# Kernel optimization log

Hardware: AMD Instinct MI355X
Metric: run time of the kernel (lower is better)

## Reference

```python
import jax, jax.numpy as jnp
import numpy as np

LATENT = 64
HID = 64
IN_DIM = HID + 1  # 65
SLOPE = 0.2
EPS = 1e-8


def setup_inputs() -> dict:
    key = jax.random.key(0)
    ks = jax.random.split(key, 9)
    x = jax.random.normal(ks[0], (8192, LATENT, IN_DIM), dtype=jnp.float32)
    def init_w(k, shape, fan_in):
        return jax.random.uniform(k, shape, jnp.float32, -1.0, 1.0) / np.sqrt(fan_in)
    # Per-latent stacked MLP params: 3 LeakyReLU layers + final linear to scalar
    W0 = init_w(ks[1], (LATENT, HID, IN_DIM), IN_DIM)
    b0 = init_w(ks[2], (LATENT, HID), IN_DIM)
    W1 = init_w(ks[3], (LATENT, HID, HID), HID)
    b1 = init_w(ks[4], (LATENT, HID), HID)
    W2 = init_w(ks[5], (LATENT, HID, HID), HID)
    b2 = init_w(ks[6], (LATENT, HID), HID)
    W3 = init_w(ks[7], (LATENT, 1, HID), HID)
    b3 = init_w(ks[8], (LATENT, 1), HID)
    return {"x": x, "W0": W0, "b0": b0, "W1": W1, "b1": b1,
            "W2": W2, "b2": b2, "W3": W3, "b3": b3}


def _flow_single(w0, b0, w1, b1, w2, b2, w3, b3, xi):
    # xi: [B, IN_DIM] -> residual [B], d(out)/d(xi[:, -1]) [B]
    def f(z):
        h = jax.nn.leaky_relu(z @ w0.T + b0, SLOPE)
        h = jax.nn.leaky_relu(h @ w1.T + b1, SLOPE)
        h = jax.nn.leaky_relu(h @ w2.T + b2, SLOPE)
        return h @ w3.T + b3  # [B, 1]
    # only the last column of the Jacobian is used -> single batched JVP
    tan = jnp.zeros_like(xi).at[:, -1].set(1.0)
    out, dout = jax.jvp(f, (xi,), (tan,))
    return out[:, 0], dout[:, 0]


def reference(x, W0, b0, W1, b1, W2, b2, W3, b3):
    B = x.shape[0]
    # vmap over the latent axis (independent MLP per latent)
    residuals, dJ = jax.vmap(_flow_single,
                             in_axes=(0, 0, 0, 0, 0, 0, 0, 0, 1),
                             out_axes=(1, 1))(W0, b0, W1, b1, W2, b2, W3, b3, x)
    # residuals: [B, LATENT]; dJ: [B, LATENT]
    logabsdet = jnp.sum(jnp.log(jnp.abs(dJ) + EPS), axis=1)  # [B]
    return residuals.reshape(B, -1), logabsdet.reshape(B, -1)
```

## Files before the change

kernel.cpp:

```cpp
#include <hip/hip_runtime.h>
#include <hip/hip_bf16.h>
#include <cmath>

#define LATENTS 64
#define HID 64
#define IN_DIM 65
#define SLOPE 0.2f
#define FEPS 1e-8f
#define RPB 128
#define WBYTES 53248
#define W65_BYTE (64 * WBYTES)

#define A_OF_SLOT(s) ((((((s) >> 2) & 1) * 2 + ((s) >> 5)) * 16) + ((((s) >> 3) & 3) * 4) + ((s) & 3))

typedef __attribute__((ext_vector_type(8))) short short8;
typedef __attribute__((ext_vector_type(4))) float f32x4;
typedef __attribute__((address_space(1))) const unsigned GASU;
typedef __attribute__((address_space(3))) unsigned LASU;

__device__ __forceinline__ unsigned asu(float f){ return __builtin_bit_cast(unsigned, f); }
__device__ __forceinline__ float    asf(unsigned u){ return __builtin_bit_cast(float, u); }
__device__ __forceinline__ unsigned bfu(float f){
    return (unsigned)__builtin_bit_cast(unsigned short, __float2bfloat16(f));
}

__device__ __forceinline__ void split8v(const float* f, short8& hi, short8& lo){
    unsigned hw[4], lw[4];
#pragma unroll
    for (int w = 0; w < 4; ++w){
        float a = f[2 * w], b = f[2 * w + 1];
        unsigned ha = asu(a) & 0xFFFF0000u, hb = asu(b) & 0xFFFF0000u;
        float la = a - asf(ha), lb = b - asf(hb);
        hw[w] = (ha >> 16) | hb;
        lw[w] = bfu(la) | (bfu(lb) << 16);
    }
    uint4 h4{hw[0], hw[1], hw[2], hw[3]}, l4{lw[0], lw[1], lw[2], lw[3]};
    hi = __builtin_bit_cast(short8, h4);
    lo = __builtin_bit_cast(short8, l4);
}

__device__ __forceinline__ void split8t(const float* f, short8& hi, short8& lo){
    unsigned hw[4], lw[4];
#pragma unroll
    for (int w = 0; w < 4; ++w){
        float a = f[2 * w], b = f[2 * w + 1];
        unsigned ha = asu(a) & 0xFFFF0000u, hb = asu(b) & 0xFFFF0000u;
        float la = a - asf(ha), lb = b - asf(hb);
        hw[w] = __builtin_amdgcn_perm(asu(b),  asu(a),  0x07060302u);
        lw[w] = __builtin_amdgcn_perm(asu(lb), asu(la), 0x07060302u);
    }
    uint4 h4{hw[0], hw[1], hw[2], hw[3]}, l4{lw[0], lw[1], lw[2], lw[3]};
    hi = __builtin_bit_cast(short8, h4);
    lo = __builtin_bit_cast(short8, l4);
}

__device__ __forceinline__ short8 pack8t(const float* f){
    unsigned w[4];
#pragma unroll
    for (int i = 0; i < 4; ++i)
        w[i] = __builtin_amdgcn_perm(asu(f[2 * i + 1]), asu(f[2 * i]), 0x07060302u);
    uint4 p{w[0], w[1], w[2], w[3]};
    return __builtin_bit_cast(short8, p);
}

__device__ __forceinline__ f32x4 mfma_(short8 a, short8 b, f32x4 c){
    return __builtin_amdgcn_mfma_f32_16x16x32_bf16(a, b, c, 0, 0, 0);
}

__global__ void lad_init_kernel(float* __restrict__ lad, int n){
    int i = blockIdx.x * blockDim.x + threadIdx.x;
    if (i < n) lad[i] = 0.0f;
}

__global__ __launch_bounds__(64)
void w_prep_kernel(const float* __restrict__ W0, const float* __restrict__ W1,
                   const float* __restrict__ W2, const float* __restrict__ W3,
                   char* __restrict__ ws)
{
    const int b = blockIdx.x;
    const int L = threadIdx.x;
    const int c  = L & 15;
    const int kb = (L >> 4) * 8;
    if (b < 192){
        const int l = b / 3, d = b - 3 * l;
        const float* Wd = (d == 0) ? W0 + (size_t)l * 64 * IN_DIM
                        : (d == 1) ? W1 + (size_t)l * 4096
                                   : W2 + (size_t)l * 4096;
        const int K = (d == 0) ? IN_DIM : 64;
#pragma unroll
        for (int ks = 0; ks < 2; ++ks)
#pragma unroll
            for (int ct = 0; ct < 4; ++ct){
                float wf[8];
#pragma unroll
                for (int j = 0; j < 8; ++j){
                    const int s = ks * 32 + kb + j;
                    const int a = (d == 0) ? s : A_OF_SLOT(s);
                    wf[j] = Wd[(size_t)(ct * 16 + c) * K + a];
                }
                short8 wh, wl;
                split8v(wf, wh, wl);
                char* base = ws + (size_t)l * WBYTES + d * 16384 + (ks * 4 + ct) * 1024 + L * 16;
                *(short8*)base            = wh;
                *(short8*)(base + 8192)   = wl;
            }
    } else {
        const int l = b - 192;
#pragma unroll
        for (int ks = 0; ks < 2; ++ks){
            float wf[8];
#pragma unroll
            for (int j = 0; j < 8; ++j)
                wf[j] = (c == 0) ? W3[l * 64 + A_OF_SLOT(ks * 32 + kb + j)] : 0.0f;
            short8 wh, wl;
            split8v(wf, wh, wl);
            char* base = ws + (size_t)l * WBYTES + 49152 + ks * 1024 + L * 16;
            *(short8*)base          = wh;
            *(short8*)(base + 2048) = wl;
        }
        ((float*)(ws + W65_BYTE))[l * 64 + L] =
            W0[(size_t)l * 64 * IN_DIM + L * IN_DIM + 64];
    }
}

__global__ __launch_bounds__(512, 4)
void flow_mfma_kernel(const float* __restrict__ x,
                      const float* __restrict__ b0, const float* __restrict__ b1,
                      const float* __restrict__ b2, const float* __restrict__ b3,
                      const char* __restrict__ ws,
                      float* __restrict__ out_res, float* __restrict__ out_lad)
{
    __shared__ __attribute__((aligned(16))) char wlds[WBYTES];

    const int l   = blockIdx.y;
    const int tid = threadIdx.x;
    const int L   = tid & 63;
    const int wv  = tid >> 6;
    const int u   = L >> 4;
    const int g0  = blockIdx.x * RPB + wv * 16 + (L & 15);

    const char* gsrc = ws + (size_t)l * WBYTES;
#pragma unroll
    for (int i = 0; i < 7; ++i){
        const int base = i * 512 + wv * 64;
        if (base * 16 < WBYTES)
            __builtin_amdgcn_global_load_lds((GASU*)(gsrc + (base + L) * 16),
                                             (LASU*)(wlds + base * 16), 16, 0, 0);
    }

    const float* xg0 = x + ((size_t)g0 * LATENTS + l) * IN_DIM;
    float xv[16];
    float x65r;
#pragma unroll
    for (int j = 0; j < 8; ++j){
        xv[j]     = xg0[8 * u + j];
        xv[8 + j] = xg0[32 + 8 * u + j];
    }
    x65r = xg0[64];

    short8 bh[2], bl2[2], th2[2];
    split8t(&xv[0], bh[0], bl2[0]);
    split8t(&xv[8], bh[1], bl2[1]);

    __syncthreads();

    f32x4 ha[4], ta[4];

    auto ldw = [&](int d, int ks, int ct, short8& wh, short8& wl){
        const char* p = wlds + d * 16384 + (ks * 4 + ct) * 1024 + (L << 4);
        wh = *(const short8*)p;
        wl = *(const short8*)(p + 8192);
    };
    auto repack = [&](const float v[4][4], short8 (&hi)[2], short8 (&lo)[2]){
#pragma unroll
        for (int ks = 0; ks < 2; ++ks){
            float f8[8] = {v[ks][0], v[ks][1], v[ks][2], v[ks][3],
                           v[2 + ks][0], v[2 + ks][1], v[2 + ks][2], v[2 + ks][3]};
            split8t(f8, hi[ks], lo[ks]);
        }
    };
    auto repackt = [&](const float v[4][4], short8 (&hi)[2]){
#pragma unroll
        for (int ks = 0; ks < 2; ++ks){
            float f8[8] = {v[ks][0], v[ks][1], v[ks][2], v[ks][3],
                           v[2 + ks][0], v[2 + ks][1], v[2 + ks][2], v[2 + ks][3]};
            hi[ks] = pack8t(f8);
        }
    };

    {
#pragma unroll
        for (int ct = 0; ct < 4; ++ct)
            ha[ct] = __builtin_bit_cast(f32x4,
                        *(const float4*)(b0 + l * 64 + ct * 16 + u * 4));
#pragma unroll
        for (int ks = 0; ks < 2; ++ks){
#pragma unroll
            for (int ct = 0; ct < 4; ++ct){
                short8 wh, wl;
                ldw(0, ks, ct, wh, wl);
                __builtin_amdgcn_s_setprio(1);
                ha[ct] = mfma_(wh, bh[ks],  ha[ct]);
                ha[ct] = mfma_(wh, bl2[ks], ha[ct]);
                ha[ct] = mfma_(wl, bh[ks],  ha[ct]);
                __builtin_amdgcn_s_setprio(0);
            }
        }
        const float* w65p = (const float*)(ws + W65_BYTE) + l * 64;
        float hv[4][4], tv[4][4];
#pragma unroll
        for (int ct = 0; ct < 4; ++ct){
            const float4 wv4 = *(const float4*)(w65p + ct * 16 + u * 4);
            const float wa[4] = {wv4.x, wv4.y, wv4.z, wv4.w};
#pragma unroll
            for (int i = 0; i < 4; ++i){
                float z = fmaf(x65r, wa[i], ha[ct][i]);
                float m = (z >= 0.0f) ? 1.0f : SLOPE;
                hv[ct][i] = z * m;
                tv[ct][i] = wa[i] * m;
            }
        }
        repack(hv, bh, bl2);
        repackt(tv, th2);
    }

    auto dense2 = [&](int d, const float* __restrict__ bl){
#pragma unroll
        for (int ct = 0; ct < 4; ++ct){
            ha[ct] = __builtin_bit_cast(f32x4,
                        *(const float4*)(bl + ct * 16 + u * 4));
            ta[ct] = (f32x4){0.f, 0.f, 0.f, 0.f};
        }
#pragma unroll
        for (int ks = 0; ks < 2; ++ks){
#pragma unroll
            for (int ct = 0; ct < 4; ++ct){
                short8 wh, wl;
                ldw(d, ks, ct, wh, wl);
                __builtin_amdgcn_s_setprio(1);
                ha[ct] = mfma_(wh, bh[ks],  ha[ct]);
                ha[ct] = mfma_(wh, bl2[ks], ha[ct]);
                ha[ct] = mfma_(wl, bh[ks],  ha[ct]);
                ta[ct] = mfma_(wh, th2[ks], ta[ct]);
                ta[ct] = mfma_(wl, th2[ks], ta[ct]);
                __builtin_amdgcn_s_setprio(0);
            }
        }
        float hv[4][4], tv[4][4];
#pragma unroll
        for (int ct = 0; ct < 4; ++ct)
#pragma unroll
            for (int i = 0; i < 4; ++i){
                float z  = ha[ct][i];
                float zt = ta[ct][i];
                float m  = (z >= 0.0f) ? 1.0f : SLOPE;
                hv[ct][i] = z * m;
                tv[ct][i] = zt * m;
            }
        repack(hv, bh, bl2);
        repackt(tv, th2);
    };
    dense2(1, b1 + l * 64);
    dense2(2, b2 + l * 64);

    {
        f32x4 so = (f32x4){0.f, 0.f, 0.f, 0.f};
        f32x4 sd = (f32x4){0.f, 0.f, 0.f, 0.f};
#pragma unroll
        for (int ks = 0; ks < 2; ++ks){
            const char* p = wlds + 49152 + ks * 1024 + (L << 4);
            short8 wh = *(const short8*)p;
            short8 wl = *(const short8*)(p + 2048);
            __builtin_amdgcn_s_setprio(1);
            so = mfma_(wh, bh[ks],  so);
            so = mfma_(wh, bl2[ks], so);
            so = mfma_(wl, bh[ks],  so);
            sd = mfma_(wh, th2[ks], sd);
            sd = mfma_(wl, th2[ks], sd);
            __builtin_amdgcn_s_setprio(0);
        }
        if (u == 0){
            out_res[(size_t)g0 * LATENTS + l] = so[0] + b3[l];
            atomicAdd(&out_lad[g0], __logf(fabsf(sd[0]) + FEPS));
        }
    }
}

extern "C" void kernel_launch(void* const* d_in, const int* in_sizes, int n_in,
                              void* d_out, int out_size, void* d_ws, size_t ws_size,
                              hipStream_t stream)
{
    const float* x  = (const float*)d_in[0];
    const float* W0 = (const float*)d_in[1];
    const float* b0 = (const float*)d_in[2];
    const float* W1 = (const float*)d_in[3];
    const float* b1 = (const float*)d_in[4];
    const float* W2 = (const float*)d_in[5];
    const float* b2 = (const float*)d_in[6];
    const float* W3 = (const float*)d_in[7];
    const float* b3 = (const float*)d_in[8];

    const int B = in_sizes[0] / (LATENTS * IN_DIM);
    float* out_res = (float*)d_out;
    float* out_lad = out_res + (size_t)B * LATENTS;
    char*  wsp     = (char*)d_ws;

    lad_init_kernel<<<dim3((B + 255) / 256), dim3(256), 0, stream>>>(out_lad, B);
    w_prep_kernel<<<dim3(256), dim3(64), 0, stream>>>(W0, W1, W2, W3, wsp);
    flow_mfma_kernel<<<dim3(B / RPB, LATENTS), dim3(512), 0, stream>>>(
        x, b0, b1, b2, b3, wsp, out_res, out_lad);
}
```

Before: 73.85 us.

## Loop each block over several row chunks and drop tangent low-part MFMAs

Each block now loads its latent's weights into LDS once and then processes 8 chunks of 128 rows in a loop, so the grid shrinks by 8x and the per-block weight staging is amortized. The tangent path now uses a single round-to-nearest bf16 operand instead of a hi/lo split, which removes one MFMA per tile in the hidden and output layers. The split helpers also switch to rounding rather than truncation. The cost is less parallelism (512 blocks in total) and a small loss of tangent precision, which could affect the log-determinant accuracy.

Result: slower. 75.42 us (+2.1%).

```diff
diff --git a/kernel.cpp b/kernel.cpp
--- a/kernel.cpp
+++ b/kernel.cpp
@@ -8,6 +8,7 @@
 #define SLOPE 0.2f
 #define FEPS 1e-8f
 #define RPB 128
+#define CHUNKS 8
 #define WBYTES 53248
 #define W65_BYTE (64 * WBYTES)
 
@@ -29,9 +30,9 @@
 #pragma unroll
     for (int w = 0; w < 4; ++w){
         float a = f[2 * w], b = f[2 * w + 1];
-        unsigned ha = asu(a) & 0xFFFF0000u, hb = asu(b) & 0xFFFF0000u;
-        float la = a - asf(ha), lb = b - asf(hb);
-        hw[w] = (ha >> 16) | hb;
+        unsigned ua = bfu(a), ub = bfu(b);
+        float la = a - asf(ua << 16), lb = b - asf(ub << 16);
+        hw[w] = ua | (ub << 16);
         lw[w] = bfu(la) | (bfu(lb) << 16);
     }
     uint4 h4{hw[0], hw[1], hw[2], hw[3]}, l4{lw[0], lw[1], lw[2], lw[3]};
@@ -44,21 +45,22 @@
 #pragma unroll
     for (int w = 0; w < 4; ++w){
         float a = f[2 * w], b = f[2 * w + 1];
-        unsigned ha = asu(a) & 0xFFFF0000u, hb = asu(b) & 0xFFFF0000u;
-        float la = a - asf(ha), lb = b - asf(hb);
-        hw[w] = __builtin_amdgcn_perm(asu(b),  asu(a),  0x07060302u);
-        lw[w] = __builtin_amdgcn_perm(asu(lb), asu(la), 0x07060302u);
+        float la = a - asf(asu(a) & 0xFFFF0000u);
+        float lb = b - asf(asu(b) & 0xFFFF0000u);
+        hw[w] = __builtin_amdgcn_perm(asu(b), asu(a), 0x07060302u);
+        lw[w] = __builtin_amdgcn_perm(asu(lb) + 0x8000u, asu(la) + 0x8000u, 0x07060302u);
     }
     uint4 h4{hw[0], hw[1], hw[2], hw[3]}, l4{lw[0], lw[1], lw[2], lw[3]};
     hi = __builtin_bit_cast(short8, h4);
     lo = __builtin_bit_cast(short8, l4);
 }
 
-__device__ __forceinline__ short8 pack8t(const float* f){
+__device__ __forceinline__ short8 pack8r(const float* f){
     unsigned w[4];
 #pragma unroll
     for (int i = 0; i < 4; ++i)
-        w[i] = __builtin_amdgcn_perm(asu(f[2 * i + 1]), asu(f[2 * i]), 0x07060302u);
+        w[i] = __builtin_amdgcn_perm(asu(f[2 * i + 1]) + 0x8000u,
+                                     asu(f[2 * i])     + 0x8000u, 0x07060302u);
     uint4 p{w[0], w[1], w[2], w[3]};
     return __builtin_bit_cast(short8, p);
 }
@@ -137,7 +139,6 @@
     const int L   = tid & 63;
     const int wv  = tid >> 6;
     const int u   = L >> 4;
-    const int g0  = blockIdx.x * RPB + wv * 16 + (L & 15);
 
     const char* gsrc = ws + (size_t)l * WBYTES;
 #pragma unroll
@@ -147,141 +148,143 @@
             __builtin_amdgcn_global_load_lds((GASU*)(gsrc + (base + L) * 16),
                                              (LASU*)(wlds + base * 16), 16, 0, 0);
     }
-
-    const float* xg0 = x + ((size_t)g0 * LATENTS + l) * IN_DIM;
-    float xv[16];
-    float x65r;
-#pragma unroll
-    for (int j = 0; j < 8; ++j){
-        xv[j]     = xg0[8 * u + j];
-        xv[8 + j] = xg0[32 + 8 * u + j];
-    }
-    x65r = xg0[64];
-
-    short8 bh[2], bl2[2], th2[2];
-    split8t(&xv[0], bh[0], bl2[0]);
-    split8t(&xv[8], bh[1], bl2[1]);
-
     __syncthreads();
-
-    f32x4 ha[4], ta[4];
 
     auto ldw = [&](int d, int ks, int ct, short8& wh, short8& wl){
         const char* p = wlds + d * 16384 + (ks * 4 + ct) * 1024 + (L << 4);
         wh = *(const short8*)p;
         wl = *(const short8*)(p + 8192);
     };
-    auto repack = [&](const float v[4][4], short8 (&hi)[2], short8 (&lo)[2]){
-#pragma unroll
-        for (int ks = 0; ks < 2; ++ks){
-            float f8[8] = {v[ks][0], v[ks][1], v[ks][2], v[ks][3],
-                           v[2 + ks][0], v[2 + ks][1], v[2 + ks][2], v[2 + ks][3]};
-            split8t(f8, hi[ks], lo[ks]);
+
+#pragma unroll 1
+    for (int it = 0; it < CHUNKS; ++it){
+        const int g0 = (blockIdx.x * CHUNKS + it) * RPB + wv * 16 + (L & 15);
+
+        const float* xg0 = x + ((size_t)g0 * LATENTS + l) * IN_DIM;
+        float xv[16];
+#pragma unroll
+        for (int j = 0; j < 8; ++j){
+            xv[j]     = xg0[8 * u + j];
+            xv[8 + j] = xg0[32 + 8 * u + j];
         }
-    };
-    auto repackt = [&](const float v[4][4], short8 (&hi)[2]){
-#pragma unroll
-        for (int ks = 0; ks < 2; ++ks){
-            float f8[8] = {v[ks][0], v[ks][1], v[ks][2], v[ks][3],
-                           v[2 + ks][0], v[2 + ks][1], v[2 + ks][2], v[2 + ks][3]};
-            hi[ks] = pack8t(f8);
+        const float x65r = xg0[64];
+
+        short8 bh[2], bl2[2], th2[2];
+        split8t(&xv[0], bh[0], bl2[0]);
+        split8t(&xv[8], bh[1], bl2[1]);
+
+        f32x4 ha[4], ta[4];
+
+        auto repack = [&](const float v[4][4], short8 (&hi)[2], short8 (&lo)[2]){
+#pragma unroll
+            for (int ks = 0; ks < 2; ++ks){
+                float f8[8] = {v[ks][0], v[ks][1], v[ks][2], v[ks][3],
+                               v[2 + ks][0], v[2 + ks][1], v[2 + ks][2], v[2 + ks][3]};
+                split8t(f8, hi[ks], lo[ks]);
+            }
+        };
+        auto repackt = [&](const float v[4][4], short8 (&hi)[2]){
+#pragma unroll
+            for (int ks = 0; ks < 2; ++ks){
+                float f8[8] = {v[ks][0], v[ks][1], v[ks][2], v[ks][3],
+                               v[2 + ks][0], v[2 + ks][1], v[2 + ks][2], v[2 + ks][3]};
+                hi[ks] = pack8r(f8);
+            }
+        };
+
+        {
+#pragma unroll
+            for (int ct = 0; ct < 4; ++ct)
+                ha[ct] = __builtin_bit_cast(f32x4,
+                            *(const float4*)(b0 + l * 64 + ct * 16 + u * 4));
+#pragma unroll
+            for (int ks = 0; ks < 2; ++ks){
+#pragma unroll
+                for (int ct = 0; ct < 4; ++ct){
+                    short8 wh, wl;
+                    ldw(0, ks, ct, wh, wl);
+                    __builtin_amdgcn_s_setprio(1);
+                    ha[ct] = mfma_(wh, bh[ks],  ha[ct]);
+                    ha[ct] = mfma_(wh, bl2[ks], ha[ct]);
+                    ha[ct] = mfma_(wl, bh[ks],  ha[ct]);
+                    __builtin_amdgcn_s_setprio(0);
+                }
+            }
+            const float* w65p = (const float*)(ws + W65_BYTE) + l * 64;
+            float hv[4][4], tv[4][4];
+#pragma unroll
+            for (int ct = 0; ct < 4; ++ct){
+                const float4 wv4 = *(const float4*)(w65p + ct * 16 + u * 4);
+                const float wa[4] = {wv4.x, wv4.y, wv4.z, wv4.w};
+#pragma unroll
+                for (int i = 0; i < 4; ++i){
+                    float z = fmaf(x65r, wa[i], ha[ct][i]);
+                    float m = (z >= 0.0f) ? 1.0f : SLOPE;
+                    hv[ct][i] = z * m;
+                    tv[ct][i] = wa[i] * m;
+                }
+            }
+            repack(hv, bh, bl2);
+            repackt(tv, th2);
         }
-    };
-
-    {
-#pragma unroll
-        for (int ct = 0; ct < 4; ++ct)
-            ha[ct] = __builtin_bit_cast(f32x4,
-                        *(const float4*)(b0 + l * 64 + ct * 16 + u * 4));
-#pragma unroll
-        for (int ks = 0; ks < 2; ++ks){
+
+        auto dense2 = [&](int d, const float* __restrict__ bl){
 #pragma unroll
             for (int ct = 0; ct < 4; ++ct){
-                short8 wh, wl;
-                ldw(0, ks, ct, wh, wl);
+                ha[ct] = __builtin_bit_cast(f32x4,
+                            *(const float4*)(bl + ct * 16 + u * 4));
+                ta[ct] = (f32x4){0.f, 0.f, 0.f, 0.f};
+            }
+#pragma unroll
+            for (int ks = 0; ks < 2; ++ks){
+#pragma unroll
+                for (int ct = 0; ct < 4; ++ct){
+                    short8 wh, wl;
+                    ldw(d, ks, ct, wh, wl);
+                    __builtin_amdgcn_s_setprio(1);
+                    ha[ct] = mfma_(wh, bh[ks],  ha[ct]);
+                    ha[ct] = mfma_(wh, bl2[ks], ha[ct]);
+                    ha[ct] = mfma_(wl, bh[ks],  ha[ct]);
+                    ta[ct] = mfma_(wh, th2[ks], ta[ct]);
+                    __builtin_amdgcn_s_setprio(0);
+                }
+            }
+            float hv[4][4], tv[4][4];
+#pragma unroll
+            for (int ct = 0; ct < 4; ++ct)
+#pragma unroll
+                for (int i = 0; i < 4; ++i){
+                    float z  = ha[ct][i];
+                    float zt = ta[ct][i];
+                    float m  = (z >= 0.0f) ? 1.0f : SLOPE;
+                    hv[ct][i] = z * m;
+                    tv[ct][i] = zt * m;
+                }
+            repack(hv, bh, bl2);
+            repackt(tv, th2);
+        };
+        dense2(1, b1 + l * 64);
+        dense2(2, b2 + l * 64);
+
+        {
+            f32x4 so = (f32x4){0.f, 0.f, 0.f, 0.f};
+            f32x4 sd = (f32x4){0.f, 0.f, 0.f, 0.f};
+#pragma unroll
+            for (int ks = 0; ks < 2; ++ks){
+                const char* p = wlds + 49152 + ks * 1024 + (L << 4);
+                short8 wh = *(const short8*)p;
+                short8 wl = *(const short8*)(p + 2048);
                 __builtin_amdgcn_s_setprio(1);
-                ha[ct] = mfma_(wh, bh[ks],  ha[ct]);
-                ha[ct] = mfma_(wh, bl2[ks], ha[ct]);
-                ha[ct] = mfma_(wl, bh[ks],  ha[ct]);
+                so = mfma_(wh, bh[ks],  so);
+                so = mfma_(wh, bl2[ks], so);
+                so = mfma_(wl, bh[ks],  so);
+                sd = mfma_(wh, th2[ks], sd);
                 __builtin_amdgcn_s_setprio(0);
             }
-        }
-        const float* w65p = (const float*)(ws + W65_BYTE) + l * 64;
-        float hv[4][4], tv[4][4];
-#pragma unroll
-        for (int ct = 0; ct < 4; ++ct){
-            const float4 wv4 = *(const float4*)(w65p + ct * 16 + u * 4);
-            const float wa[4] = {wv4.x, wv4.y, wv4.z, wv4.w};
-#pragma unroll
-            for (int i = 0; i < 4; ++i){
-                float z = fmaf(x65r, wa[i], ha[ct][i]);
-                float m = (z >= 0.0f) ? 1.0f : SLOPE;
-                hv[ct][i] = z * m;
-                tv[ct][i] = wa[i] * m;
-            }
-        }
-        repack(hv, bh, bl2);
-        repackt(tv, th2);
-    }
-
-    auto dense2 = [&](int d, const float* __restrict__ bl){
-#pragma unroll
-        for (int ct = 0; ct < 4; ++ct){
-            ha[ct] = __builtin_bit_cast(f32x4,
-                        *(const float4*)(bl + ct * 16 + u * 4));
-            ta[ct] = (f32x4){0.f, 0.f, 0.f, 0.f};
-        }
-#pragma unroll
-        for (int ks = 0; ks < 2; ++ks){
-#pragma unroll
-            for (int ct = 0; ct < 4; ++ct){
-                short8 wh, wl;
-                ldw(d, ks, ct, wh, wl);
-                __builtin_amdgcn_s_setprio(1);
-                ha[ct] = mfma_(wh, bh[ks],  ha[ct]);
-                ha[ct] = mfma_(wh, bl2[ks], ha[ct]);
-                ha[ct] = mfma_(wl, bh[ks],  ha[ct]);
-                ta[ct] = mfma_(wh, th2[ks], ta[ct]);
-                ta[ct] = mfma_(wl, th2[ks], ta[ct]);
-                __builtin_amdgcn_s_setprio(0);
-            }
-        }
-        float hv[4][4], tv[4][4];
-#pragma unroll
-        for (int ct = 0; ct < 4; ++ct)
-#pragma unroll
-            for (int i = 0; i < 4; ++i){
-                float z  = ha[ct][i];
-                float zt = ta[ct][i];
-                float m  = (z >= 0.0f) ? 1.0f : SLOPE;
-                hv[ct][i] = z * m;
-                tv[ct][i] = zt * m;
-            }
-        repack(hv, bh, bl2);
-        repackt(tv, th2);
-    };
-    dense2(1, b1 + l * 64);
-    dense2(2, b2 + l * 64);
-
-    {
-        f32x4 so = (f32x4){0.f, 0.f, 0.f, 0.f};
-        f32x4 sd = (f32x4){0.f, 0.f, 0.f, 0.f};
-#pragma unroll
-        for (int ks = 0; ks < 2; ++ks){
-            const char* p = wlds + 49152 + ks * 1024 + (L << 4);
-            short8 wh = *(const short8*)p;
-            short8 wl = *(const short8*)(p + 2048);
-            __builtin_amdgcn_s_setprio(1);
-            so = mfma_(wh, bh[ks],  so);
-            so = mfma_(wh, bl2[ks], so);
-            so = mfma_(wl, bh[ks],  so);
-            sd = mfma_(wh, th2[ks], sd);
-            sd = mfma_(wl, th2[ks], sd);
-            __builtin_amdgcn_s_setprio(0);
-        }
-        if (u == 0){
-            out_res[(size_t)g0 * LATENTS + l] = so[0] + b3[l];
-            atomicAdd(&out_lad[g0], __logf(fabsf(sd[0]) + FEPS));
+            if (u == 0){
+                out_res[(size_t)g0 * LATENTS + l] = so[0] + b3[l];
+                atomicAdd(&out_lad[g0], __logf(fabsf(sd[0]) + FEPS));
+            }
         }
     }
 }
@@ -307,6 +310,6 @@
 
     lad_init_kernel<<<dim3((B + 255) / 256), dim3(256), 0, stream>>>(out_lad, B);
     w_prep_kernel<<<dim3(256), dim3(64), 0, stream>>>(W0, W1, W2, W3, wsp);
-    flow_mfma_kernel<<<dim3(B / RPB, LATENTS), dim3(512), 0, stream>>>(
+    flow_mfma_kernel<<<dim3(B / (RPB * CHUNKS), LATENTS), dim3(512), 0, stream>>>(
         x, b0, b1, b2, b3, wsp, out_res, out_lad);
 }
```
